# Kernel tuning notes

Hardware: AMD Instinct MI355X
Metric: run time of the kernel (lower is better)

## Reference

```python
import jax, jax.numpy as jnp
import numpy as np

B = 262144
H = 128  # h_dim == embedding_dim
S = 128  # social_feat_size
IN_DIM = 8  # abs_rel


def setup_inputs() -> dict:
    key = jax.random.key(0)
    ks = jax.random.split(key, 16)
    sc = 0.05
    return {
        "xy": jax.random.normal(ks[0], (B, 4), jnp.float32),
        "dxdy": jax.random.normal(ks[1], (B, 4), jnp.float32),
        "social_feats": jax.random.normal(ks[2], (B, S), jnp.float32),
        "h0": jax.random.normal(ks[3], (1, B, H), jnp.float32),
        "pred_len": 12,
        # spatial_embedding: Linear(8 -> 128)
        "emb_W": jax.random.normal(ks[4], (H, IN_DIM), jnp.float32) * sc,
        "emb_b": jax.random.normal(ks[5], (H,), jnp.float32) * sc,
        # GRU (single layer): gate order r,z,n as in torch
        "W_ih": jax.random.normal(ks[6], (3 * H, H), jnp.float32) * sc,
        "W_hh": jax.random.normal(ks[7], (3 * H, H), jnp.float32) * sc,
        "b_ih": jax.random.normal(ks[8], (3 * H,), jnp.float32) * sc,
        "b_hh": jax.random.normal(ks[9], (3 * H,), jnp.float32) * sc,
        # hidden2pos MLP: [h_dim + social, h_dim//2, 4], leaky_relu after each Linear
        "W1": jax.random.normal(ks[10], (H // 2, H + S), jnp.float32) * sc,
        "b1": jax.random.normal(ks[11], (H // 2,), jnp.float32) * sc,
        "W2": jax.random.normal(ks[12], (4, H // 2), jnp.float32) * sc,
        "b2": jax.random.normal(ks[13], (4,), jnp.float32) * sc,
    }


def _gru_cell(x, h, W_ih, W_hh, b_ih, b_hh):
    gi = x @ W_ih.T + b_ih  # (B, 3H)
    gh = h @ W_hh.T + b_hh
    i_r, i_z, i_n = jnp.split(gi, 3, axis=-1)
    h_r, h_z, h_n = jnp.split(gh, 3, axis=-1)
    r = jax.nn.sigmoid(i_r + h_r)
    z = jax.nn.sigmoid(i_z + h_z)
    n = jnp.tanh(i_n + r * h_n)
    return (1.0 - z) * n + z * h


def reference(xy, dxdy, social_feats, h0, pred_len, emb_W, emb_b,
              W_ih, W_hh, b_ih, b_hh, W1, b1, W2, b2):
    last_obsv0 = jnp.concatenate([xy, dxdy], axis=1)  # (B, 8)
    h_init = h0[0]  # single layer -> (B, H)

    def step(carry, _):
        last_obsv, h = carry
        x = last_obsv @ emb_W.T + emb_b            # spatial embedding (abs_rel: full 8 dims)
        h = _gru_cell(x, h, W_ih, W_hh, b_ih, b_hh)
        inp = jnp.concatenate([h, social_feats], axis=1)
        z1 = jax.nn.leaky_relu(inp @ W1.T + b1)    # LeakyReLU(0.01) per make_mlp
        new_dxdy = jax.nn.leaky_relu(z1 @ W2.T + b2)  # (B, 4)
        wh = last_obsv[:, 2:4] * jnp.exp(new_dxdy[:, 2:4])      # new w,h
        xy_new = last_obsv[:, :2] + new_dxdy[:, :2] - 0.5 * wh  # shift by half w,h
        new_obsv = jnp.concatenate([xy_new, wh, new_dxdy], axis=1)
        return (new_obsv, h), new_obsv

    _, preds = jax.lax.scan(step, (last_obsv0, h_init), None, length=pred_len)
    return preds[:, :, :4], preds[:, :, 4:]
```

## Files before the change

### kernel.cpp

```cpp
#include <hip/hip_runtime.h>

typedef _Float16 half_t;
typedef _Float16 half8 __attribute__((ext_vector_type(8)));
typedef float f32x4 __attribute__((ext_vector_type(4)));
typedef float f32x2 __attribute__((ext_vector_type(2)));

#define B_TOT    262144
#define PRED_LEN 12
#define NBLK     (B_TOT/64)

#define OFF_WHH 0
#define OFF_WC  49152
#define OFF_W1S 61440
#define OFF_W1H 69632
#define OFF_W2  77824
#define HALFS_TOTAL 78848
#define NFLOATS 196
#define PREP_TOTAL (HALFS_TOTAL + NFLOATS)

#define A_RZ (-1.44269504f)
#define A_N  (2.88539008f)

#define K32(a,b,c) __builtin_amdgcn_mfma_f32_16x16x32_f16((a),(b),(c),0,0,0)

__device__ __forceinline__ float exp2f_(float x){ return __builtin_amdgcn_exp2f(x); }
__device__ __forceinline__ float rcpf_(float x){ return __builtin_amdgcn_rcpf(x); }

__global__ void prep_kernel(const float* __restrict__ emb_W, const float* __restrict__ emb_b,
                            const float* __restrict__ W_ih, const float* __restrict__ W_hh,
                            const float* __restrict__ b_ih, const float* __restrict__ b_hh,
                            const float* __restrict__ W1,   const float* __restrict__ W2,
                            const float* __restrict__ b1,   const float* __restrict__ b2,
                            half_t* __restrict__ wsh, float* __restrict__ wsf) {
  int f = blockIdx.x*256 + threadIdx.x;
  if (f >= PREP_TOTAL) return;
  if (f < OFF_WC) {
    int e=f&7, l=(f>>3)&63, c=(f>>9)&3, ct=f>>11;
    int g=ct>>3, jb=ct&7;
    int col=g*128+jb*16+(l&15);
    int k=c*32+(l>>4)*8+e;
    float a=(g<2)?A_RZ:A_N;
    wsh[f]=(half_t)(a*W_hh[col*128+k]);
  } else if (f < OFF_W1S) {
    int ff=f-OFF_WC;
    int e=ff&7, l=(ff>>3)&63, ct=ff>>9;
    int g=ct>>3, jb=ct&7;
    int col=g*128+jb*16+(l&15);
    int sub=l>>4;
    float a=(g<2)?A_RZ:A_N;
    float v=0.f;
    if (sub<=1) {
      float wc=0.f;
      for (int m=0;m<128;++m) wc = fmaf(W_ih[col*128+m], emb_W[m*8+e], wc);
      v = a*64.f*wc;
      if (sub==1) v *= (1.f/2048.f);
    } else if (sub==2 && e==0) {
      float bi=b_ih[col];
      for (int m=0;m<128;++m) bi = fmaf(W_ih[col*128+m], emb_b[m], bi);
      if (g<2) bi += b_hh[col];
      v = a*bi;
    }
    wsh[f]=(half_t)v;
  } else if (f < OFF_W1H) {
    int ff=f-OFF_W1S;
    int e=ff&7, l=(ff>>3)&63, c=(ff>>9)&3, ct=ff>>11;
    int col=ct*16+(l&15);
    int k=c*32+(l>>4)*8+e;
    wsh[f]=(half_t)W1[col*256 + 128 + k];
  } else if (f < OFF_W2) {
    int ff=f-OFF_W1H;
    int e=ff&7, l=(ff>>3)&63, c=(ff>>9)&3, ct=ff>>11;
    int col=ct*16+(l&15);
    int k=c*32+(l>>4)*8+e;
    wsh[f]=(half_t)W1[col*256 + k];
  } else if (f < HALFS_TOTAL) {
    int ff=f-OFF_W2;
    int e=ff&7, l=(ff>>3)&63, c=ff>>9;
    int col=l&15;
    int k=c*32+(l>>4)*8+e;
    wsh[f]=(half_t)((col<4)?W2[col*64+k]:0.f);
  } else {
    int ff=f-HALFS_TOTAL;
    float v;
    if (ff < 64)       v = b1[ff];
    else if (ff < 192) v = A_N*b_hh[256 + (ff-64)];
    else               v = b2[ff-192];
    wsf[ff]=v;
  }
}

__device__ __forceinline__ void write_split(half_t* obsplit, int row, int s, float v){
  float scv = v * 0.015625f;
  half_t hi = (half_t)scv;
  float lo = (scv - (float)hi) * 2048.0f;
  obsplit[row*16 + s]     = hi;
  obsplit[row*16 + 8 + s] = (half_t)lo;
}

__device__ __forceinline__ void stage_tile(const float* __restrict__ src, half_t* htile,
                                           int b0, int tid){
  int row = tid>>3, cg = (tid&7)*16;
  const float* s = src + (size_t)(b0+row)*128 + cg;
  half8 p0, p1;
#pragma unroll
  for (int i=0;i<8;++i) p0[i] = (half_t)s[i];
#pragma unroll
  for (int i=0;i<8;++i) p1[i] = (half_t)s[8+i];
  int base = cg>>3;
  *(half8*)&htile[row*128 + (( base    ^ (row&15))<<3)] = p0;
  *(half8*)&htile[row*128 + (((base+1) ^ (row&15))<<3)] = p1;
}

__global__ __launch_bounds__(512, 2)
void decoder_kernel(const float* __restrict__ xy, const float* __restrict__ dxdy,
                    const float* __restrict__ social, const float* __restrict__ h0,
                    const half_t* __restrict__ wsh, const float* __restrict__ wsf,
                    float* __restrict__ out) {
  __shared__ half_t buf0[64*128], buf1[64*128];
  __shared__ half_t w1h_lds[8192];
  __shared__ half_t w2_lds[1024];
  __shared__ half_t z1t[64*64];
  __shared__ half_t obsplit[64*16];
  __shared__ float  obsf[64*4];

  const int tid = threadIdx.x;
  const int wid = tid>>6, lane = tid&63;
  const int l15 = lane&15, l4 = lane>>4;
  const int b0 = blockIdx.x*64;

  half8 Bg[3][4];
  half8 Bi[3];
#pragma unroll
  for (int g=0; g<3; ++g){
#pragma unroll
    for (int c=0;c<4;++c)
      Bg[g][c] = *(const half8*)(wsh + OFF_WHH + ((size_t)((g*8+wid)*4+c)*64 + lane)*8);
    Bi[g] = *(const half8*)(wsh + OFF_WC + ((size_t)(g*8+wid)*64 + lane)*8);
  }
  const int mycol = wid*16 + l15;
  const float bHN = wsf[64 + mycol];

  for (int i = tid; i < 1024; i += 512)
    *(half8*)&w1h_lds[i*8] = *(const half8*)(wsh + OFF_W1H + (size_t)i*8);
  if (tid < 128)
    *(half8*)&w2_lds[tid*8] = *(const half8*)(wsh + OFF_W2 + (size_t)tid*8);

  stage_tile(social, buf0, b0, tid);
  __syncthreads();

  float sc[2][4];
  {
    int Mt = wid>>1;
    int arow = Mt*16 + l15;
    half8 ha[4];
#pragma unroll
    for (int c=0;c<4;++c){
      int slot = (c*4 + l4) ^ (arow&15);
      ha[c] = *(const half8*)&buf0[arow*128 + slot*8];
    }
#pragma unroll
    for (int c2=0;c2<2;++c2){
      int ct = (wid&1)*2 + c2;
      float b1v = wsf[ct*16 + l15];
      f32x4 acc = {b1v,b1v,b1v,b1v};
#pragma unroll
      for (int c=0;c<4;++c){
        half8 bw = *(const half8*)(wsh + OFF_W1S + ((size_t)(ct*4+c)*64 + lane)*8);
        acc = K32(ha[c], bw, acc);
      }
#pragma unroll
      for (int r=0;r<4;++r) sc[c2][r] = acc[r];
    }
  }
  __syncthreads();

  stage_tile(h0, buf0, b0, tid);
  if (tid < 256) {
    int row = tid>>2, q = tid&3;
    size_t gb = (size_t)(b0+row)*4;
    if (q < 2) {
      float vx = xy[gb+q], vw = xy[gb+q+2];
      write_split(obsplit, row, q,   vx);
      write_split(obsplit, row, q+2, vw);
      obsf[row*4 + q]     = vx;
      obsf[row*4 + q + 2] = vw;
    } else {
      int c0 = (q-2)*2;
      write_split(obsplit, row, 4+c0, dxdy[gb+c0]);
      write_split(obsplit, row, 5+c0, dxdy[gb+c0+1]);
    }
  }
  float hq[4][4];
#pragma unroll
  for (int Mt=0;Mt<4;++Mt)
#pragma unroll
    for (int r=0;r<4;++r)
      hq[Mt][r] = h0[(size_t)(b0 + Mt*16 + l4*4 + r)*128 + mycol];
  __syncthreads();

  float* out0 = out;
  float* out1 = out + (size_t)PRED_LEN*B_TOT*4;

#pragma unroll 1
  for (int t=0; t<PRED_LEN; ++t) {
    const half_t* rb = (t&1) ? buf1 : buf0;
    half_t*       wb = (t&1) ? buf0 : buf1;

#pragma unroll
    for (int Mt=0; Mt<4; ++Mt) {
      int arow = Mt*16 + l15;
      half8 oa = {0,0,0,0,0,0,0,0};
      if (lane < 32)      oa = *(const half8*)&obsplit[arow*16 + l4*8];
      else if (lane < 48) oa[0] = (half_t)1.f;
      f32x4 ar  = {0.f,0.f,0.f,0.f};
      f32x4 az  = {0.f,0.f,0.f,0.f};
      f32x4 ain = {0.f,0.f,0.f,0.f};
      f32x4 ahn = {bHN,bHN,bHN,bHN};
      ar  = K32(oa, Bi[0], ar);
      az  = K32(oa, Bi[1], az);
      ain = K32(oa, Bi[2], ain);
      half8 ha0 = *(const half8*)&rb[arow*128 + (((0*4+l4)^(arow&15))<<3)];
      half8 ha1 = *(const half8*)&rb[arow*128 + (((1*4+l4)^(arow&15))<<3)];
      ar  = K32(ha0, Bg[0][0], ar);  az  = K32(ha0, Bg[1][0], az);  ahn = K32(ha0, Bg[2][0], ahn);
      ar  = K32(ha1, Bg[0][1], ar);  az  = K32(ha1, Bg[1][1], az);  ahn = K32(ha1, Bg[2][1], ahn);
      half8 ha2 = *(const half8*)&rb[arow*128 + (((2*4+l4)^(arow&15))<<3)];
      half8 ha3 = *(const half8*)&rb[arow*128 + (((3*4+l4)^(arow&15))<<3)];
      ar  = K32(ha2, Bg[0][2], ar);  az  = K32(ha2, Bg[1][2], az);  ahn = K32(ha2, Bg[2][2], ahn);
      ar  = K32(ha3, Bg[0][3], ar);  az  = K32(ha3, Bg[1][3], az);  ahn = K32(ha3, Bg[2][3], ahn);
#pragma unroll
      for (int r=0;r<4;++r){
        float R  = rcpf_(1.f + exp2f_(ar[r]));
        float Z  = rcpf_(1.f + exp2f_(az[r]));
        float np = fmaf(R, ahn[r], ain[r]);
        float N  = 1.f - 2.f*rcpf_(exp2f_(np) + 1.f);
        float h  = N + Z*(hq[Mt][r] - N);
        hq[Mt][r] = h;
        int hrow = Mt*16 + l4*4 + r;
        wb[hrow*128 + (((mycol>>3)^(hrow&15))<<3) + (mycol&7)] = (half_t)h;
      }
    }
    __syncthreads();

    {
      int Mt = wid>>1;
      int arow = Mt*16 + l15;
      half8 ha[4];
#pragma unroll
      for (int c=0;c<4;++c){
        int slot = (c*4+l4) ^ (arow&15);
        ha[c] = *(const half8*)&wb[arow*128 + slot*8];
      }
#pragma unroll
      for (int c2=0;c2<2;++c2){
        int ct = (wid&1)*2 + c2;
        f32x4 acc = {sc[c2][0], sc[c2][1], sc[c2][2], sc[c2][3]};
#pragma unroll
        for (int c=0;c<4;++c){
          half8 bw = *(const half8*)&w1h_lds[((ct*4+c)*64 + lane)*8];
          acc = K32(ha[c], bw, acc);
        }
        int col = ct*16 + l15;
#pragma unroll
        for (int r=0;r<4;++r){
          int zrow = Mt*16 + l4*4 + r;
          float v = acc[r];
          v = fmaxf(v, 0.01f*v);
          z1t[zrow*64 + (((col>>3)^(zrow&7))<<3) + (col&7)] = (half_t)v;
        }
      }
    }
    __syncthreads();

    if (wid < 4) {
      int Mt = wid;
      int arow = Mt*16 + l15;
      half8 za0 = *(const half8*)&z1t[arow*64 + (((0*4+l4)^(arow&7))<<3)];
      half8 za1 = *(const half8*)&z1t[arow*64 + (((1*4+l4)^(arow&7))<<3)];
      half8 w2f0 = *(const half8*)&w2_lds[(0*64+lane)*8];
      half8 w2f1 = *(const half8*)&w2_lds[(1*64+lane)*8];
      float b2l = (l15<4) ? wsf[192+l15] : 0.f;
      f32x4 acc = {b2l,b2l,b2l,b2l};
      acc = K32(za0, w2f0, acc);
      acc = K32(za1, w2f1, acc);
      float d[4], dx1[4], dx2[4], dx3[4];
#pragma unroll
      for (int r=0;r<4;++r){
        float v = acc[r];
        d[r] = fmaxf(v, 0.01f*v);
      }
#pragma unroll
      for (int r=0;r<4;++r){
        dx1[r] = __shfl_xor(d[r], 1);
        dx2[r] = __shfl_xor(d[r], 2);
        dx3[r] = __shfl_xor(d[r], 3);
      }
      if (l15 < 4) {
        int q = l15;
#pragma unroll
        for (int r=0;r<4;++r){
          int row = Mt*16 + l4*4 + r;
          size_t ob = (size_t)((size_t)t*B_TOT + b0 + row)*4;
          if (q < 2) {
            float x = obsf[row*4 + q];
            float w = obsf[row*4 + q + 2];
            float wh = w * exp2f_(dx2[r] * 1.44269504f);
            float xn = x + d[r] - 0.5f*wh;
            obsf[row*4 + q]     = xn;
            obsf[row*4 + q + 2] = wh;
            out0[ob + q]     = xn;
            out0[ob + q + 2] = wh;
            write_split(obsplit, row, q,   xn);
            write_split(obsplit, row, q+2, wh);
          } else if (q == 2) {
            f32x2 v = {dx2[r], dx3[r]};
            *(f32x2*)&out1[ob + 0] = v;
            write_split(obsplit, row, 4, dx2[r]);
            write_split(obsplit, row, 5, dx3[r]);
          } else {
            f32x2 v = {dx1[r], d[r]};
            *(f32x2*)&out1[ob + 2] = v;
            write_split(obsplit, row, 6, dx1[r]);
            write_split(obsplit, row, 7, d[r]);
          }
        }
      }
    }
    __syncthreads();
  }
}

extern "C" void kernel_launch(void* const* d_in, const int* in_sizes, int n_in,
                              void* d_out, int out_size, void* d_ws, size_t ws_size,
                              hipStream_t stream) {
  const float* xy     = (const float*)d_in[0];
  const float* dxdy   = (const float*)d_in[1];
  const float* social = (const float*)d_in[2];
  const float* h0     = (const float*)d_in[3];
  const float* emb_W  = (const float*)d_in[5];
  const float* emb_b  = (const float*)d_in[6];
  const float* W_ih   = (const float*)d_in[7];
  const float* W_hh   = (const float*)d_in[8];
  const float* b_ih   = (const float*)d_in[9];
  const float* b_hh   = (const float*)d_in[10];
  const float* W1     = (const float*)d_in[11];
  const float* b1     = (const float*)d_in[12];
  const float* W2     = (const float*)d_in[13];
  const float* b2     = (const float*)d_in[14];

  half_t* wsh = (half_t*)d_ws;
  float*  wsf = (float*)((char*)d_ws + (size_t)HALFS_TOTAL*2);

  prep_kernel<<<(PREP_TOTAL+255)/256, 256, 0, stream>>>(
      emb_W, emb_b, W_ih, W_hh, b_ih, b_hh, W1, W2, b1, b2, wsh, wsf);
  decoder_kernel<<<NBLK, 512, 0, stream>>>(
      xy, dxdy, social, h0, wsh, wsf, (float*)d_out);
}
```

Measured before the change: 841.0 us.

## Merge hidden-MLP and output layers per wave pair, dropping a barrier

```diff
diff --git a/kernel.cpp b/kernel.cpp
--- a/kernel.cpp
+++ b/kernel.cpp
@@ -93,8 +93,8 @@
   float scv = v * 0.015625f;
   half_t hi = (half_t)scv;
   float lo = (scv - (float)hi) * 2048.0f;
-  obsplit[row*16 + s]     = hi;
-  obsplit[row*16 + 8 + s] = (half_t)lo;
+  obsplit[row*20 + s]     = hi;
+  obsplit[row*20 + 8 + s] = (half_t)lo;
 }
 
 __device__ __forceinline__ void stage_tile(const float* __restrict__ src, half_t* htile,
@@ -111,16 +111,16 @@
   *(half8*)&htile[row*128 + (((base+1) ^ (row&15))<<3)] = p1;
 }
 
-__global__ __launch_bounds__(512, 2)
+__global__ __launch_bounds__(512, 4)
 void decoder_kernel(const float* __restrict__ xy, const float* __restrict__ dxdy,
                     const float* __restrict__ social, const float* __restrict__ h0,
                     const half_t* __restrict__ wsh, const float* __restrict__ wsf,
                     float* __restrict__ out) {
   __shared__ half_t buf0[64*128], buf1[64*128];
   __shared__ half_t w1h_lds[8192];
-  __shared__ half_t w2_lds[1024];
-  __shared__ half_t z1t[64*64];
-  __shared__ half_t obsplit[64*16];
+  __shared__ half_t z1t[4*16*64];
+  __shared__ float  scf[64*64];
+  __shared__ half_t obsplit[64*20];
   __shared__ float  obsf[64*4];
 
   const int tid = threadIdx.x;
@@ -139,16 +139,13 @@
   }
   const int mycol = wid*16 + l15;
   const float bHN = wsf[64 + mycol];
+  const float b2l = (l15<4) ? wsf[192+l15] : 0.f;
 
   for (int i = tid; i < 1024; i += 512)
     *(half8*)&w1h_lds[i*8] = *(const half8*)(wsh + OFF_W1H + (size_t)i*8);
-  if (tid < 128)
-    *(half8*)&w2_lds[tid*8] = *(const half8*)(wsh + OFF_W2 + (size_t)tid*8);
 
   stage_tile(social, buf0, b0, tid);
   __syncthreads();
-
-  float sc[2][4];
   {
     int Mt = wid>>1;
     int arow = Mt*16 + l15;
@@ -161,15 +158,16 @@
 #pragma unroll
     for (int c2=0;c2<2;++c2){
       int ct = (wid&1)*2 + c2;
-      float b1v = wsf[ct*16 + l15];
+      int col = ct*16 + l15;
+      float b1v = wsf[col];
       f32x4 acc = {b1v,b1v,b1v,b1v};
 #pragma unroll
       for (int c=0;c<4;++c){
         half8 bw = *(const half8*)(wsh + OFF_W1S + ((size_t)(ct*4+c)*64 + lane)*8);
         acc = K32(ha[c], bw, acc);
       }
-#pragma unroll
-      for (int r=0;r<4;++r) sc[c2][r] = acc[r];
+      int slot = (Mt*4 + l4) ^ (col&15);
+      *(f32x4*)&scf[col*64 + slot*4] = acc;
     }
   }
   __syncthreads();
@@ -210,7 +208,7 @@
     for (int Mt=0; Mt<4; ++Mt) {
       int arow = Mt*16 + l15;
       half8 oa = {0,0,0,0,0,0,0,0};
-      if (lane < 32)      oa = *(const half8*)&obsplit[arow*16 + l4*8];
+      if (lane < 32)      oa = *(const half8*)&obsplit[arow*20 + l4*8];
       else if (lane < 48) oa[0] = (half_t)1.f;
       f32x4 ar  = {0.f,0.f,0.f,0.f};
       f32x4 az  = {0.f,0.f,0.f,0.f};
@@ -242,50 +240,44 @@
     __syncthreads();
 
     {
-      int Mt = wid>>1;
-      int arow = Mt*16 + l15;
+      const int m = wid>>1, p = wid&1;
+      half8 w2f0 = *(const half8*)(wsh + OFF_W2 + (size_t)(0*64+lane)*8);
+      half8 w2f1 = *(const half8*)(wsh + OFF_W2 + (size_t)(1*64+lane)*8);
+      int arow = m*16 + l15;
       half8 ha[4];
 #pragma unroll
       for (int c=0;c<4;++c){
         int slot = (c*4+l4) ^ (arow&15);
         ha[c] = *(const half8*)&wb[arow*128 + slot*8];
       }
-#pragma unroll
-      for (int c2=0;c2<2;++c2){
-        int ct = (wid&1)*2 + c2;
-        f32x4 acc = {sc[c2][0], sc[c2][1], sc[c2][2], sc[c2][3]};
+      half_t* zt = z1t + m*1024;
+#pragma unroll
+      for (int ct=0; ct<4; ++ct){
+        int col = ct*16 + l15;
+        int slot = (m*4 + l4) ^ (col&15);
+        f32x4 acc = *(const f32x4*)&scf[col*64 + slot*4];
 #pragma unroll
         for (int c=0;c<4;++c){
           half8 bw = *(const half8*)&w1h_lds[((ct*4+c)*64 + lane)*8];
           acc = K32(ha[c], bw, acc);
         }
-        int col = ct*16 + l15;
 #pragma unroll
         for (int r=0;r<4;++r){
-          int zrow = Mt*16 + l4*4 + r;
+          int zrow = l4*4 + r;
           float v = acc[r];
           v = fmaxf(v, 0.01f*v);
-          z1t[zrow*64 + (((col>>3)^(zrow&7))<<3) + (col&7)] = (half_t)v;
+          zt[zrow*64 + (((col>>3)^(zrow&7))<<3) + (col&7)] = (half_t)v;
         }
       }
-    }
-    __syncthreads();
-
-    if (wid < 4) {
-      int Mt = wid;
-      int arow = Mt*16 + l15;
-      half8 za0 = *(const half8*)&z1t[arow*64 + (((0*4+l4)^(arow&7))<<3)];
-      half8 za1 = *(const half8*)&z1t[arow*64 + (((1*4+l4)^(arow&7))<<3)];
-      half8 w2f0 = *(const half8*)&w2_lds[(0*64+lane)*8];
-      half8 w2f1 = *(const half8*)&w2_lds[(1*64+lane)*8];
-      float b2l = (l15<4) ? wsf[192+l15] : 0.f;
-      f32x4 acc = {b2l,b2l,b2l,b2l};
-      acc = K32(za0, w2f0, acc);
-      acc = K32(za1, w2f1, acc);
+      half8 za0 = *(const half8*)&zt[l15*64 + (((0*4+l4)^(l15&7))<<3)];
+      half8 za1 = *(const half8*)&zt[l15*64 + (((1*4+l4)^(l15&7))<<3)];
+      f32x4 wacc = {b2l,b2l,b2l,b2l};
+      wacc = K32(za0, w2f0, wacc);
+      wacc = K32(za1, w2f1, wacc);
       float d[4], dx1[4], dx2[4], dx3[4];
 #pragma unroll
       for (int r=0;r<4;++r){
-        float v = acc[r];
+        float v = wacc[r];
         d[r] = fmaxf(v, 0.01f*v);
       }
 #pragma unroll
@@ -298,7 +290,8 @@
         int q = l15;
 #pragma unroll
         for (int r=0;r<4;++r){
-          int row = Mt*16 + l4*4 + r;
+          if ((r>>1) != p) continue;
+          int row = m*16 + l4*4 + r;
           size_t ob = (size_t)((size_t)t*B_TOT + b0 + row)*4;
           if (q < 2) {
             float x = obsf[row*4 + q];
```

Measured after the change: 2.006 ms. +138.6%, slower.
